# Kernel tuning notes

Measured on AMD Instinct MI355X. Metric: run time of the kernel, lower is better.

Reference implementation:

```python
import jax, jax.numpy as jnp
import numpy as np

B, L, H = 64, 512, 512          # batch, max_len, hidden_size (code requires H == L)
ITEM = 50001                    # item_num + 1
TEMP = 0.2                      # gumbel-sigmoid temperature
EPS = 1e-20


def setup_inputs() -> dict:
    key = jax.random.key(0)
    ks = jax.random.split(key, 16)
    lin = lambda k: jax.random.normal(k, (L, L), jnp.float32) * (1.0 / np.sqrt(L))
    U = jax.random.uniform(ks[13], (L, H), jnp.float32)
    gumbel = -jnp.log(-jnp.log(U + EPS) + EPS)
    return {
        "positives": jax.random.randint(ks[0], (B, L), 0, ITEM),
        "mask": jax.random.randint(ks[1], (B, L), 0, 2).astype(jnp.int32),
        "item_emb": jax.random.normal(ks[2], (ITEM, H), jnp.float32) * 0.02,
        "pos_emb": jax.random.normal(ks[3], (L, H), jnp.float32) * 0.02,
        "Wz": lin(ks[4]),
        "Wv": lin(ks[5]),
        "Wq": lin(ks[6]),
        "Wk": lin(ks[7]),
        "gamma_q": jax.random.normal(ks[8], (L,), jnp.float32) * 0.02,
        "beta_q": jnp.zeros((L,), jnp.float32),
        "gamma_k": jax.random.normal(ks[9], (L,), jnp.float32) * 0.02,
        "beta_k": jnp.zeros((L,), jnp.float32),
        "sparse_w": jax.random.uniform(ks[10], (L, H), jnp.float32, 0.2, 0.8),
        "gumbel": gumbel,
    }


def reference(positives, mask, item_emb, pos_emb, Wz, Wv, Wq, Wk,
              gamma_q, beta_q, gamma_k, beta_k, sparse_w, gumbel):
    # ---- merge_attn_masks: True = masked ----
    pad = ~(mask.astype(bool))[:, None, :]                 # [B,1,L]
    future = jnp.triu(jnp.ones((L, L), bool), k=1)         # strictly upper
    merged = pad | future[None]                            # [B,L,L]
    attn_mask = (~jnp.eye(L, dtype=bool))[None] & merged   # keep diagonal unmasked

    # ---- embeddings ----
    x = item_emb[positives] + pos_emb[None]                # [B,L,H]

    # ---- GAU-style projections (Linear acts on last dim, y = x @ W^T) ----
    z = jax.nn.silu(x @ Wz.T)                              # [B,L,H]
    v = jax.nn.silu(x @ Wv.T)                              # [B,L,H]
    q = (z @ Wq.T) * gamma_q + beta_q                      # OffsetScale head 0
    k = (z @ Wk.T) * gamma_k + beta_k

    # ---- relu^2 attention with bool mask added then zeroed ----
    m = attn_mask.astype(q.dtype)
    a = jnp.einsum('bld,bmd->blm', q, k) + m               # torch adds bool as 0/1
    a = a * (1.0 - m)                                      # a * ~attn_mask

    # ---- gumbel-sigmoid sparse mask (broadcast [L,L] over batch) ----
    smask = jax.nn.sigmoid((jnp.log(sparse_w / (1.0 - sparse_w)) + gumbel) / TEMP)
    a = smask[None] * a

    a = jnp.square(jax.nn.relu(a)) / (L * H)
    return a @ v                                           # [B,L,H]
```

## Files before the change

kernel.cpp:

```cpp
#include <hip/hip_runtime.h>
#include <hip/hip_fp16.h>
#include <math.h>

typedef _Float16 f16;
typedef unsigned int u32;
typedef _Float16 f16x8 __attribute__((ext_vector_type(8)));
typedef _Float16 f16x4 __attribute__((ext_vector_type(4)));
typedef float    f32x4 __attribute__((ext_vector_type(4)));

constexpr int LEN  = 512;
constexpr int HID  = 512;
constexpr int BATCH = 64;

__device__ __forceinline__ void gload16(const f16* g, f16* l) {
    __builtin_amdgcn_global_load_lds((const __attribute__((address_space(1))) u32*)g,
                                     (__attribute__((address_space(3))) u32*)l,
                                     16, 0, 0);
}

__device__ __forceinline__ float silu_f(float v) {
    return v * __builtin_amdgcn_rcpf(1.f + __expf(-v));
}

#define TP 16384
#define EP 264

__device__ __forceinline__ void stage_pass(const f16* __restrict__ g, f16* l) {
    const int tid = threadIdx.x;
    const int row = tid >> 2;
    const int sc  = (tid & 3) ^ ((row >> 1) & 3);
    gload16(g + (size_t)row * 512 + sc * 8, l + (tid >> 6) * 512);
}

__device__ __forceinline__ void stage_tile(const f16* __restrict__ A,
                                           const f16* __restrict__ B,
                                           int t, f16* buf) {
    stage_pass(A + t * 32,             buf);
    stage_pass(A + t * 32 + 128 * 512, buf + 4096);
    stage_pass(B + t * 32,             buf + 8192);
    stage_pass(B + t * 32 + 128 * 512, buf + 12288);
}

__device__ __forceinline__ void gemm8p(const f16* __restrict__ A,
                                       const f16* __restrict__ B,
                                       int nt, f16* lds, f32x4 acc[8][4])
{
    const int lane = threadIdx.x & 63;
    const int wv   = threadIdx.x >> 6;
    const int wr = wv >> 2, wc = wv & 3;
    const int mf = lane & 15;
    const int slot = ((lane >> 4) ^ ((mf >> 1) & 3)) * 8;
    const int abase = wr * 4096 + mf * 32 + slot;
    const int bbase = 8192 + (wc >> 1) * 4096 + ((wc & 1) * 64 + mf) * 32 + slot;

    #pragma unroll
    for (int m = 0; m < 8; ++m)
        #pragma unroll
        for (int n = 0; n < 4; ++n)
            acc[m][n] = (f32x4){0.f, 0.f, 0.f, 0.f};

    stage_tile(A, B, 0, lds);
    stage_tile(A, B, 1, lds + TP);
    stage_tile(A, B, 2, lds + 2 * TP);
    asm volatile("s_waitcnt vmcnt(8)" ::: "memory");
    __builtin_amdgcn_s_barrier();

    for (int t = 0; t < nt; ++t) {
        f16* buf  = lds + (t & 3) * TP;
        f16* nbuf = lds + ((t + 3) & 3) * TP;
        const bool st = (t + 3 < nt);
        f16x8 af[4], bf[4];

        #pragma unroll
        for (int m = 0; m < 4; ++m) af[m] = *(const f16x8*)(buf + abase + m * 512);
        #pragma unroll
        for (int n = 0; n < 4; ++n) bf[n] = *(const f16x8*)(buf + bbase + n * 512);
        if (st) {
            stage_pass(A + (t + 3) * 32,             nbuf);
            stage_pass(A + (t + 3) * 32 + 128 * 512, nbuf + 4096);
        }
        __builtin_amdgcn_s_barrier();
        asm volatile("s_waitcnt lgkmcnt(0)" ::: "memory");
        __builtin_amdgcn_sched_barrier(0);
        __builtin_amdgcn_s_setprio(1);
        #pragma unroll
        for (int m = 0; m < 4; ++m)
            #pragma unroll
            for (int n = 0; n < 4; ++n)
                acc[m][n] = __builtin_amdgcn_mfma_f32_16x16x32_f16(af[m], bf[n], acc[m][n], 0, 0, 0);
        __builtin_amdgcn_s_setprio(0);
        __builtin_amdgcn_s_barrier();

        #pragma unroll
        for (int m = 0; m < 4; ++m) af[m] = *(const f16x8*)(buf + abase + (m + 4) * 512);
        if (st) {
            stage_pass(B + (t + 3) * 32,             nbuf + 8192);
            stage_pass(B + (t + 3) * 32 + 128 * 512, nbuf + 12288);
        }
        __builtin_amdgcn_s_barrier();
        asm volatile("s_waitcnt lgkmcnt(0)" ::: "memory");
        __builtin_amdgcn_sched_barrier(0);
        __builtin_amdgcn_s_setprio(1);
        #pragma unroll
        for (int m = 0; m < 4; ++m)
            #pragma unroll
            for (int n = 0; n < 4; ++n)
                acc[m + 4][n] = __builtin_amdgcn_mfma_f32_16x16x32_f16(af[m], bf[n], acc[m + 4][n], 0, 0, 0);
        __builtin_amdgcn_s_setprio(0);
        if (t < nt - 3)       { asm volatile("s_waitcnt vmcnt(8)" ::: "memory"); }
        else if (t == nt - 3) { asm volatile("s_waitcnt vmcnt(4)" ::: "memory"); }
        else if (t == nt - 2) { asm volatile("s_waitcnt vmcnt(0)" ::: "memory"); }
        __builtin_amdgcn_s_barrier();
    }
}

#define EPI_IDX() \
    const int lane = threadIdx.x & 63, wv_ = threadIdx.x >> 6;  \
    const int wr = wv_ >> 2, wc = wv_ & 3;                      \
    const int c0 = lane & 15, r0 = (lane >> 4) * 4;

__device__ __forceinline__ void copy_half(const f16* lds, f16* __restrict__ gout,
                                          int ldo, int h) {
    const int tid = threadIdx.x;
    #pragma unroll
    for (int ph = 0; ph < 8; ++ph) {
        const int r = ph * 16 + (tid >> 5);
        const int c = (tid & 31) * 8;
        *(f16x8*)(gout + (size_t)(h * 128 + r) * ldo + c) = *(const f16x8*)(lds + r * EP + c);
    }
}

__global__ __launch_bounds__(512, 2) void k_zv8(const f16* __restrict__ x,
                                                const f16* __restrict__ Wzh,
                                                const f16* __restrict__ Wvh,
                                                f16* __restrict__ z,
                                                f16* __restrict__ vt)
{
    __shared__ __align__(16) f16 lds[4 * TP];
    const int bid = blockIdx.x;
    const int s  = (bid & 7) + 8 * (bid >> 5);
    const int ci = (bid >> 3) & 3;
    const f16* A; const f16* Bm; f16* gout;
    if (ci < 2) {
        A = x + (size_t)s * 256 * HID;
        Bm = Wzh + (size_t)ci * 256 * HID;
        gout = z + (size_t)s * 256 * HID + ci * 256;
    } else {
        const int ht = ci - 2;
        A = Wvh + (size_t)ht * 256 * HID;
        Bm = x + (size_t)s * 256 * HID;
        gout = vt + (size_t)(s >> 1) * LEN * HID + (size_t)ht * 256 * LEN + (s & 1) * 256;
    }
    f32x4 acc[8][4];
    gemm8p(A, Bm, 16, lds, acc);
    EPI_IDX();
    __syncthreads();
    #pragma unroll
    for (int h = 0; h < 2; ++h) {
        if (wr == h) {
            #pragma unroll
            for (int m = 0; m < 8; ++m)
                #pragma unroll
                for (int n = 0; n < 4; ++n)
                    #pragma unroll
                    for (int i = 0; i < 4; ++i)
                        lds[(m * 16 + r0 + i) * EP + wc * 64 + n * 16 + c0] =
                            (f16)silu_f(acc[m][n][i]);
        }
        __syncthreads();
        copy_half(lds, gout, 512, h);
        __syncthreads();
    }
}

__global__ __launch_bounds__(512, 2) void k_qkp8(const f16* __restrict__ z,
                                                 const f16* __restrict__ Wqh,
                                                 const f16* __restrict__ Wkh,
                                                 const float* __restrict__ gq,
                                                 const float* __restrict__ bq,
                                                 const float* __restrict__ gk,
                                                 const float* __restrict__ bk,
                                                 f16* __restrict__ qh,
                                                 f16* __restrict__ kh)
{
    __shared__ __align__(16) f16 lds[4 * TP];
    const int bid = blockIdx.x;
    const int s  = (bid & 7) + 8 * (bid >> 5);
    const int ci = (bid >> 3) & 3;
    const bool isq = ci < 2;
    const int ct = ci & 1;
    const f16* W = isq ? Wqh : Wkh;
    const float* g  = isq ? gq : gk;
    const float* be = isq ? bq : bk;
    f16* outp = isq ? qh : kh;
    f32x4 acc[8][4];
    gemm8p(z + (size_t)s * 256 * HID, W + (size_t)ct * 256 * HID, 16, lds, acc);
    EPI_IDX();
    f16* gbase = outp + (size_t)s * 256 * HID + ct * 256;
    __syncthreads();
    #pragma unroll
    for (int h = 0; h < 2; ++h) {
        if (wr == h) {
            #pragma unroll
            for (int n = 0; n < 4; ++n) {
                const int col = wc * 64 + n * 16 + c0;
                const int jg = ct * 256 + col;
                const float ga = g[jg], ba = be[jg];
                #pragma unroll
                for (int m = 0; m < 8; ++m)
                    #pragma unroll
                    for (int i = 0; i < 4; ++i)
                        lds[(m * 16 + r0 + i) * EP + col] =
                            (f16)((acc[m][n][i] * ga + ba) * 1024.f);
            }
        }
        __syncthreads();
        copy_half(lds, gbase, 512, h);
        __syncthreads();
    }
}

__constant__ int LT3[3] = {0, 1, 1};
__constant__ int MT3[3] = {0, 0, 1};

__global__ __launch_bounds__(512, 2) void k_qk8(const f16* __restrict__ q,
                                                const f16* __restrict__ kmat,
                                                const int* __restrict__ mask,
                                                const float* __restrict__ smask,
                                                f16* __restrict__ p)
{
    __shared__ __align__(16) f16 lds[4 * TP];
    const int bid = blockIdx.x;
    const int tt = (bid >> 3) % 3;
    const int b = (bid & 7) + 8 * (bid / 24);
    const int lt = LT3[tt], mt = MT3[tt];
    const size_t boff = (size_t)b * LEN * HID;
    f32x4 acc[8][4];
    gemm8p(q + boff + (size_t)lt * 256 * HID,
           kmat + boff + (size_t)mt * 256 * HID, 16, lds, acc);
    EPI_IDX();
    f16* gbase = p + (size_t)b * LEN * LEN + (size_t)lt * 256 * LEN + mt * 256;
    __syncthreads();
    #pragma unroll
    for (int h = 0; h < 2; ++h) {
        if (wr == h) {
            #pragma unroll
            for (int n = 0; n < 4; ++n) {
                const int col = wc * 64 + n * 16 + c0;
                const int m_g = mt * 256 + col;
                const int keepcol = mask[b * LEN + m_g];
                #pragma unroll
                for (int m = 0; m < 8; ++m)
                    #pragma unroll
                    for (int i = 0; i < 4; ++i) {
                        const int row = m * 16 + r0 + i;
                        const int l_g = lt * 256 + h * 128 + row;
                        const bool keep = (l_g == m_g) || ((m_g <= l_g) && (keepcol != 0));
                        float v = keep ? acc[m][n][i] * smask[l_g * LEN + m_g] : 0.f;
                        v = fmaxf(v, 0.f);
                        lds[row * EP + col] = (f16)(v * v);
                    }
            }
        }
        __syncthreads();
        copy_half(lds, gbase, 512, h);
        __syncthreads();
    }
}

__global__ __launch_bounds__(512, 2) void k_pv8(const f16* __restrict__ p,
                                                const f16* __restrict__ vt,
                                                float* __restrict__ out)
{
    __shared__ __align__(16) f16 lds[4 * TP];
    const int bid = blockIdx.x;
    const int inner = (bid >> 3) & 3;
    const int b = (bid & 7) + 8 * (bid >> 5);
    const int lt = 1 - (inner >> 1), ht = inner & 1;
    f32x4 acc[8][4];
    gemm8p(p + (size_t)b * LEN * LEN + (size_t)lt * 256 * LEN,
           vt + (size_t)b * HID * LEN + (size_t)ht * 256 * LEN,
           (lt + 1) * 8, lds, acc);
    EPI_IDX();
    const float SCALE = 3.4694469519536142e-18f;
    #pragma unroll
    for (int m = 0; m < 8; ++m)
        #pragma unroll
        for (int n = 0; n < 4; ++n) {
            const int h_g = ht * 256 + wc * 64 + n * 16 + c0;
            #pragma unroll
            for (int i = 0; i < 4; ++i) {
                const int l_g = lt * 256 + wr * 128 + m * 16 + r0 + i;
                out[(size_t)b * LEN * HID + (size_t)l_g * HID + h_g] = acc[m][n][i] * SCALE;
            }
        }
}

__global__ __launch_bounds__(256) void k_prep(const int* __restrict__ pos,
                                              const float* __restrict__ item_emb,
                                              const float* __restrict__ pos_emb,
                                              f16* __restrict__ x,
                                              const float* __restrict__ Wz,
                                              const float* __restrict__ Wv,
                                              const float* __restrict__ Wq,
                                              const float* __restrict__ Wk,
                                              f16* __restrict__ Wzh,
                                              f16* __restrict__ Wvh,
                                              f16* __restrict__ Wqh,
                                              f16* __restrict__ Wkh,
                                              const float* __restrict__ sw,
                                              const float* __restrict__ gum,
                                              float* __restrict__ smask)
{
    const int bid = blockIdx.x;
    const int tid = threadIdx.x;
    if (bid < 16384) {
        const int t = bid * 256 + tid;
        const int i = t >> 7;
        const int c = t & 127;
        const int l = i & (LEN - 1);
        const int item = pos[i];
        const float4 a  = ((const float4*)(item_emb + (size_t)item * HID))[c];
        const float4 b4 = ((const float4*)(pos_emb + (size_t)l * HID))[c];
        f16x4 o = { (f16)(a.x + b4.x), (f16)(a.y + b4.y),
                    (f16)(a.z + b4.z), (f16)(a.w + b4.w) };
        *(f16x4*)(x + (size_t)t * 4) = o;
    } else if (bid < 16384 + 1024) {
        const int r = bid - 16384;
        const int w = r >> 8;
        const float* s = (w == 0) ? Wz : (w == 1) ? Wv : (w == 2) ? Wq : Wk;
        f16* d = (w == 0) ? Wzh : (w == 1) ? Wvh : (w == 2) ? Wqh : Wkh;
        const int t = (r & 255) * 256 + tid;
        const float4 v = ((const float4*)s)[t];
        f16x4 o = { (f16)v.x, (f16)v.y, (f16)v.z, (f16)v.w };
        *(f16x4*)(d + (size_t)t * 4) = o;
    } else {
        const int t = (bid - 16384 - 1024) * 256 + tid;
        const float4 w4 = ((const float4*)sw)[t];
        const float4 g4 = ((const float4*)gum)[t];
        float4 o;
        o.x = __builtin_amdgcn_rcpf(1.f + __expf(-(__logf(w4.x / (1.f - w4.x)) + g4.x) * 5.f));
        o.y = __builtin_amdgcn_rcpf(1.f + __expf(-(__logf(w4.y / (1.f - w4.y)) + g4.y) * 5.f));
        o.z = __builtin_amdgcn_rcpf(1.f + __expf(-(__logf(w4.z / (1.f - w4.z)) + g4.z) * 5.f));
        o.w = __builtin_amdgcn_rcpf(1.f + __expf(-(__logf(w4.w / (1.f - w4.w)) + g4.w) * 5.f));
        ((float4*)smask)[t] = o;
    }
}

extern "C" void kernel_launch(void* const* d_in, const int* in_sizes, int n_in,
                              void* d_out, int out_size, void* d_ws, size_t ws_size,
                              hipStream_t stream)
{
    const int*   positives = (const int*)  d_in[0];
    const int*   mask      = (const int*)  d_in[1];
    const float* item_emb  = (const float*)d_in[2];
    const float* pos_emb   = (const float*)d_in[3];
    const float* Wz        = (const float*)d_in[4];
    const float* Wv        = (const float*)d_in[5];
    const float* Wq        = (const float*)d_in[6];
    const float* Wk        = (const float*)d_in[7];
    const float* gamma_q   = (const float*)d_in[8];
    const float* beta_q    = (const float*)d_in[9];
    const float* gamma_k   = (const float*)d_in[10];
    const float* beta_k    = (const float*)d_in[11];
    const float* sparse_w  = (const float*)d_in[12];
    const float* gumbel    = (const float*)d_in[13];
    float* out = (float*)d_out;

    char* ws = (char*)d_ws;
    const size_t BUFB = (size_t)BATCH * LEN * HID * sizeof(f16);
    f16* buf0 = (f16*)ws;
    f16* buf1 = (f16*)(ws + BUFB);
    f16* buf2 = (f16*)(ws + 2 * BUFB);
    f16* qh   = (f16*)(ws + 3 * BUFB);
    f16* kh   = (f16*)(ws + 4 * BUFB);
    f16* Wzh  = (f16*)(ws + 5 * BUFB);
    f16* Wvh  = Wzh + LEN * HID;
    f16* Wqh  = Wvh + LEN * HID;
    f16* Wkh  = Wqh + LEN * HID;
    float* smask = (float*)(Wkh + LEN * HID);

    k_prep<<<16384 + 1024 + 256, 256, 0, stream>>>(
        positives, item_emb, pos_emb, buf0,
        Wz, Wv, Wq, Wk, Wzh, Wvh, Wqh, Wkh,
        sparse_w, gumbel, smask);

    k_zv8<<<512, 512, 0, stream>>>(buf0, Wzh, Wvh, buf1, buf2);

    k_qkp8<<<512, 512, 0, stream>>>(buf1, Wqh, Wkh,
                                    gamma_q, beta_q, gamma_k, beta_k, qh, kh);

    k_qk8<<<192, 512, 0, stream>>>(qh, kh, mask, smask, buf0);

    k_pv8<<<256, 512, 0, stream>>>(buf0, buf2, out);
}
```

Before: 392.2 us.

## Use smaller 256x128 tiles with triple-buffered GEMM for QK and PV kernels

Adds a new GEMM core with 256x128 output tiles, 8 waves of 64x64 each, a 3-stage LDS ring and 4 blocks per CU. It replaces the 256x256 tiles in the QK^T and P·V kernels, so the grids double to 384 and 512 blocks. The aim is better load balance and occupancy on the many CUs, since the old grids (192 and 256 blocks) underfilled the machine. The cost is less operand reuse per block, so more global and LDS traffic per FLOP.

```diff
diff --git a/kernel.cpp b/kernel.cpp
--- a/kernel.cpp
+++ b/kernel.cpp
@@ -22,9 +22,6 @@
     return v * __builtin_amdgcn_rcpf(1.f + __expf(-v));
 }
 
-#define TP 16384
-#define EP 264
-
 __device__ __forceinline__ void stage_pass(const f16* __restrict__ g, f16* l) {
     const int tid = threadIdx.x;
     const int row = tid >> 2;
@@ -32,9 +29,12 @@
     gload16(g + (size_t)row * 512 + sc * 8, l + (tid >> 6) * 512);
 }
 
-__device__ __forceinline__ void stage_tile(const f16* __restrict__ A,
-                                           const f16* __restrict__ B,
-                                           int t, f16* buf) {
+#define TP 16384
+#define EP 264
+
+__device__ __forceinline__ void stage_tile4(const f16* __restrict__ A,
+                                            const f16* __restrict__ B,
+                                            int t, f16* buf) {
     stage_pass(A + t * 32,             buf);
     stage_pass(A + t * 32 + 128 * 512, buf + 4096);
     stage_pass(B + t * 32,             buf + 8192);
@@ -59,9 +59,9 @@
         for (int n = 0; n < 4; ++n)
             acc[m][n] = (f32x4){0.f, 0.f, 0.f, 0.f};
 
-    stage_tile(A, B, 0, lds);
-    stage_tile(A, B, 1, lds + TP);
-    stage_tile(A, B, 2, lds + 2 * TP);
+    stage_tile4(A, B, 0, lds);
+    stage_tile4(A, B, 1, lds + TP);
+    stage_tile4(A, B, 2, lds + 2 * TP);
     asm volatile("s_waitcnt vmcnt(8)" ::: "memory");
     __builtin_amdgcn_s_barrier();
 
@@ -114,13 +114,13 @@
     }
 }
 
-#define EPI_IDX() \
+#define EPI_IDX8() \
     const int lane = threadIdx.x & 63, wv_ = threadIdx.x >> 6;  \
     const int wr = wv_ >> 2, wc = wv_ & 3;                      \
     const int c0 = lane & 15, r0 = (lane >> 4) * 4;
 
-__device__ __forceinline__ void copy_half(const f16* lds, f16* __restrict__ gout,
-                                          int ldo, int h) {
+__device__ __forceinline__ void copy_half256(const f16* lds, f16* __restrict__ gout,
+                                             int ldo, int h) {
     const int tid = threadIdx.x;
     #pragma unroll
     for (int ph = 0; ph < 8; ++ph) {
@@ -153,7 +153,7 @@
     }
     f32x4 acc[8][4];
     gemm8p(A, Bm, 16, lds, acc);
-    EPI_IDX();
+    EPI_IDX8();
     __syncthreads();
     #pragma unroll
     for (int h = 0; h < 2; ++h) {
@@ -168,7 +168,7 @@
                             (f16)silu_f(acc[m][n][i]);
         }
         __syncthreads();
-        copy_half(lds, gout, 512, h);
+        copy_half256(lds, gout, 512, h);
         __syncthreads();
     }
 }
@@ -195,7 +195,7 @@
     f16* outp = isq ? qh : kh;
     f32x4 acc[8][4];
     gemm8p(z + (size_t)s * 256 * HID, W + (size_t)ct * 256 * HID, 16, lds, acc);
-    EPI_IDX();
+    EPI_IDX8();
     f16* gbase = outp + (size_t)s * 256 * HID + ct * 256;
     __syncthreads();
     #pragma unroll
@@ -215,82 +215,165 @@
             }
         }
         __syncthreads();
-        copy_half(lds, gbase, 512, h);
-        __syncthreads();
-    }
-}
-
-__constant__ int LT3[3] = {0, 1, 1};
-__constant__ int MT3[3] = {0, 0, 1};
-
-__global__ __launch_bounds__(512, 2) void k_qk8(const f16* __restrict__ q,
+        copy_half256(lds, gbase, 512, h);
+        __syncthreads();
+    }
+}
+
+#define TUNIT 12288
+#define EPIP  136
+
+__device__ __forceinline__ void stage_tile3(const f16* __restrict__ A,
+                                            const f16* __restrict__ B,
+                                            int kt, f16* buf) {
+    stage_pass(A + kt * 32,             buf);
+    stage_pass(A + kt * 32 + 128 * 512, buf + 4096);
+    stage_pass(B + kt * 32,             buf + 8192);
+}
+
+__device__ __forceinline__ void gemm8b(const f16* __restrict__ A,
+                                       const f16* __restrict__ B,
+                                       int ksteps, f16* lds, f32x4 acc[4][4])
+{
+    const int lane = threadIdx.x & 63;
+    const int wv   = threadIdx.x >> 6;
+    const int wr = wv >> 1, wc = wv & 1;
+    const int mf = lane & 15;
+    const int slot = ((lane >> 4) ^ ((mf >> 1) & 3)) * 8;
+    const int aoff = (wr * 64 + mf) * 32 + slot;
+    const int boff = (wc * 64 + mf) * 32 + slot + 8192;
+
+    #pragma unroll
+    for (int m = 0; m < 4; ++m)
+        #pragma unroll
+        for (int n = 0; n < 4; ++n)
+            acc[m][n] = (f32x4){0.f, 0.f, 0.f, 0.f};
+
+    stage_tile3(A, B, 0, lds);
+    stage_tile3(A, B, 1, lds + TUNIT);
+    asm volatile("s_waitcnt vmcnt(3)" ::: "memory");
+    __builtin_amdgcn_s_barrier();
+
+    int cb = 0;
+    for (int kt = 0; kt < ksteps; ++kt) {
+        f16* buf = lds + cb * TUNIT;
+        f16x8 af[4], bf[4];
+        #pragma unroll
+        for (int m = 0; m < 4; ++m) af[m] = *(const f16x8*)(buf + aoff + m * 512);
+        #pragma unroll
+        for (int n = 0; n < 4; ++n) bf[n] = *(const f16x8*)(buf + boff + n * 512);
+        if (kt + 2 < ksteps) {
+            int nb = cb + 2; if (nb >= 3) nb -= 3;
+            stage_tile3(A, B, kt + 2, lds + nb * TUNIT);
+        }
+        asm volatile("s_waitcnt lgkmcnt(0)" ::: "memory");
+        __builtin_amdgcn_sched_barrier(0);
+        __builtin_amdgcn_s_setprio(1);
+        #pragma unroll
+        for (int m = 0; m < 4; ++m)
+            #pragma unroll
+            for (int n = 0; n < 4; ++n)
+                acc[m][n] = __builtin_amdgcn_mfma_f32_16x16x32_f16(af[m], bf[n], acc[m][n], 0, 0, 0);
+        __builtin_amdgcn_s_setprio(0);
+        if (kt + 3 <= ksteps) {
+            asm volatile("s_waitcnt vmcnt(3)" ::: "memory");
+            __builtin_amdgcn_s_barrier();
+        } else if (kt + 2 == ksteps) {
+            asm volatile("s_waitcnt vmcnt(0)" ::: "memory");
+            __builtin_amdgcn_s_barrier();
+        }
+        cb = cb + 1; if (cb >= 3) cb = 0;
+    }
+}
+
+#define EPI_IDXB() \
+    const int lane = threadIdx.x & 63, wv_ = threadIdx.x >> 6;  \
+    const int wr = wv_ >> 1, wc = wv_ & 1;                      \
+    const int c0 = lane & 15, r0 = (lane >> 4) * 4;
+
+__device__ __forceinline__ void copy_half128(const f16* lds, f16* __restrict__ gout,
+                                             int ldo, int h) {
+    const int tid = threadIdx.x;
+    #pragma unroll
+    for (int ph = 0; ph < 4; ++ph) {
+        const int r = ph * 32 + (tid >> 4);
+        const int c = (tid & 15) * 8;
+        *(f16x8*)(gout + (size_t)(h * 128 + r) * ldo + c) = *(const f16x8*)(lds + r * EPIP + c);
+    }
+}
+
+__constant__ int LT6[6] = {0,0,1,1,1,1};
+__constant__ int MT6[6] = {0,1,0,1,2,3};
+
+__global__ __launch_bounds__(512, 4) void k_qk8(const f16* __restrict__ q,
                                                 const f16* __restrict__ kmat,
                                                 const int* __restrict__ mask,
                                                 const float* __restrict__ smask,
                                                 f16* __restrict__ p)
 {
-    __shared__ __align__(16) f16 lds[4 * TP];
+    __shared__ __align__(16) f16 lds[3 * TUNIT];
     const int bid = blockIdx.x;
-    const int tt = (bid >> 3) % 3;
-    const int b = (bid & 7) + 8 * (bid / 24);
-    const int lt = LT3[tt], mt = MT3[tt];
+    const int t = (bid >> 3) % 6;
+    const int b = (bid & 7) + 8 * (bid / 48);
+    const int lt = LT6[t], mt = MT6[t];
     const size_t boff = (size_t)b * LEN * HID;
-    f32x4 acc[8][4];
-    gemm8p(q + boff + (size_t)lt * 256 * HID,
-           kmat + boff + (size_t)mt * 256 * HID, 16, lds, acc);
-    EPI_IDX();
-    f16* gbase = p + (size_t)b * LEN * LEN + (size_t)lt * 256 * LEN + mt * 256;
+    f32x4 acc[4][4];
+    gemm8b(q + boff + (size_t)lt * 256 * HID,
+           kmat + boff + (size_t)mt * 128 * HID, HID / 32, lds, acc);
     __syncthreads();
+    EPI_IDXB();
+    f16* gbase = p + (size_t)b * LEN * LEN + (size_t)lt * 256 * LEN + mt * 128;
     #pragma unroll
     for (int h = 0; h < 2; ++h) {
-        if (wr == h) {
+        if ((wr >> 1) == h) {
+            const int rb = (wr & 1) * 64;
             #pragma unroll
             for (int n = 0; n < 4; ++n) {
                 const int col = wc * 64 + n * 16 + c0;
-                const int m_g = mt * 256 + col;
+                const int m_g = mt * 128 + col;
                 const int keepcol = mask[b * LEN + m_g];
                 #pragma unroll
-                for (int m = 0; m < 8; ++m)
+                for (int m = 0; m < 4; ++m)
                     #pragma unroll
                     for (int i = 0; i < 4; ++i) {
-                        const int row = m * 16 + r0 + i;
+                        const int row = rb + m * 16 + r0 + i;
                         const int l_g = lt * 256 + h * 128 + row;
                         const bool keep = (l_g == m_g) || ((m_g <= l_g) && (keepcol != 0));
                         float v = keep ? acc[m][n][i] * smask[l_g * LEN + m_g] : 0.f;
                         v = fmaxf(v, 0.f);
-                        lds[row * EP + col] = (f16)(v * v);
+                        lds[row * EPIP + col] = (f16)(v * v);
                     }
             }
         }
         __syncthreads();
-        copy_half(lds, gbase, 512, h);
-        __syncthreads();
-    }
-}
-
-__global__ __launch_bounds__(512, 2) void k_pv8(const f16* __restrict__ p,
+        copy_half128(lds, gbase, 512, h);
+        __syncthreads();
+    }
+}
+
+__global__ __launch_bounds__(512, 4) void k_pv8(const f16* __restrict__ p,
                                                 const f16* __restrict__ vt,
                                                 float* __restrict__ out)
 {
-    __shared__ __align__(16) f16 lds[4 * TP];
+    __shared__ __align__(16) f16 lds[3 * TUNIT];
     const int bid = blockIdx.x;
-    const int inner = (bid >> 3) & 3;
-    const int b = (bid & 7) + 8 * (bid >> 5);
-    const int lt = 1 - (inner >> 1), ht = inner & 1;
-    f32x4 acc[8][4];
-    gemm8p(p + (size_t)b * LEN * LEN + (size_t)lt * 256 * LEN,
-           vt + (size_t)b * HID * LEN + (size_t)ht * 256 * LEN,
+    const int inner = (bid >> 3) & 7;
+    const int b = (bid & 7) + 8 * (bid >> 6);
+    const int lt = 1 - (inner >> 2), ht = inner & 3;
+    f32x4 acc[4][4];
+    gemm8b(p + (size_t)b * LEN * LEN + (size_t)lt * 256 * LEN,
+           vt + (size_t)b * HID * LEN + (size_t)ht * 128 * LEN,
            (lt + 1) * 8, lds, acc);
-    EPI_IDX();
+    EPI_IDXB();
     const float SCALE = 3.4694469519536142e-18f;
     #pragma unroll
-    for (int m = 0; m < 8; ++m)
+    for (int m = 0; m < 4; ++m)
         #pragma unroll
         for (int n = 0; n < 4; ++n) {
-            const int h_g = ht * 256 + wc * 64 + n * 16 + c0;
+            const int h_g = ht * 128 + wc * 64 + n * 16 + c0;
             #pragma unroll
             for (int i = 0; i < 4; ++i) {
-                const int l_g = lt * 256 + wr * 128 + m * 16 + r0 + i;
+                const int l_g = lt * 256 + wr * 64 + m * 16 + r0 + i;
                 out[(size_t)b * LEN * HID + (size_t)l_g * HID + h_g] = acc[m][n][i] * SCALE;
             }
         }
@@ -390,7 +473,7 @@
     k_qkp8<<<512, 512, 0, stream>>>(buf1, Wqh, Wkh,
                                     gamma_q, beta_q, gamma_k, beta_k, qh, kh);
 
-    k_qk8<<<192, 512, 0, stream>>>(qh, kh, mask, smask, buf0);
-
-    k_pv8<<<256, 512, 0, stream>>>(buf0, buf2, out);
-}
+    k_qk8<<<384, 512, 0, stream>>>(qh, kh, mask, smask, buf0);
+
+    k_pv8<<<512, 512, 0, stream>>>(buf0, buf2, out);
+}
```

Result: faster. 371.7 us (-5.2%).
